# Performance work log

Measured on AMD Instinct MI355X. Metric: run time of the kernel, lower is better.

## Reference

```python
import jax, jax.numpy as jnp
import numpy as np

B, S, DN, L = 2048, 8, 8, 50        # batch, n_sparse, n_dense, hist len
V, VF = 100000, 100000              # sparse vocab, feed vocab
ED, FD = 16, 512                    # sparse embed dim, feed embed dim
HID1, HID2 = 256, 128               # DNN hidden sizes
NE, NT, EO = 8, 4, 8                # experts, tasks, expert out dim
INPUT_DIM = ED * S + DN + FD + FD   # 1160


def setup_inputs() -> dict:
    key = jax.random.key(0)
    ks = jax.random.split(key, 20)
    sc = 0.02
    f32 = jnp.float32
    return {
        "sparse_ids": jax.random.randint(ks[0], (B, S), 0, V),
        "dense": jax.random.normal(ks[1], (B, DN), f32),
        "feedid": jax.random.randint(ks[2], (B,), 0, VF),
        "hist_feedid": jax.random.randint(ks[3], (B, L), 0, VF),
        "emb_tables": jax.random.normal(ks[4], (S, V, ED), f32) * sc,
        "feed_table": jax.random.normal(ks[5], (VF, FD), f32) * sc,
        "attn_w1": jax.random.normal(ks[6], (4 * FD, 128), f32) * sc,
        "attn_b1": jnp.zeros((128,), f32),
        "attn_w2": jax.random.normal(ks[7], (128, 1), f32) * sc,
        "attn_b2": jnp.zeros((1,), f32),
        "dnn_w1": jax.random.normal(ks[8], (INPUT_DIM, HID1), f32) * sc,
        "dnn_b1": jnp.zeros((HID1,), f32),
        "dnn_w2": jax.random.normal(ks[9], (HID1, HID2), f32) * sc,
        "dnn_b2": jnp.zeros((HID2,), f32),
        "expert_w": jax.random.normal(ks[10], (NE, HID2, EO), f32) * sc,
        "gate_w": jax.random.normal(ks[11], (NT, HID2, NE), f32) * sc,
        "out_w": jax.random.normal(ks[12], (NT, EO, 1), f32) * sc,
        "out_b": jnp.zeros((NT, 1), f32),
    }


def reference(sparse_ids, dense, feedid, hist_feedid,
              emb_tables, feed_table,
              attn_w1, attn_b1, attn_w2, attn_b2,
              dnn_w1, dnn_b1, dnn_w2, dnn_b2,
              expert_w, gate_w, out_w, out_b):
    # --- sparse embeddings: one table per feature -> [B, S, ED] -> flat ---
    embed = jax.vmap(lambda t, ids: t[ids], in_axes=(0, 1), out_axes=1)(
        emb_tables, sparse_ids)                       # [B, S, ED]
    sparse_flat = embed.reshape(embed.shape[0], -1)   # [B, S*ED]

    # --- feed / history embeddings ---
    feed = feed_table[feedid]                         # [B, FD]
    hist = feed_table[hist_feedid]                    # [B, L, FD]

    # --- DIN attention (query=feed, keys=hist) ---
    q = jnp.broadcast_to(feed[:, None, :], hist.shape)          # [B, L, FD]
    x = jnp.concatenate([q, hist, q - hist, q * hist], axis=-1)  # [B, L, 4FD]
    h = jax.nn.relu(x @ attn_w1 + attn_b1)                       # [B, L, 128]
    scores = (h @ attn_w2 + attn_b2)[..., 0]                     # [B, L]
    attn = jax.nn.softmax(scores, axis=1)
    user_interest = jnp.einsum('bl,bld->bd', attn, hist)         # [B, FD]

    # --- DNN (dropout off in eval) ---
    dnn_in = jnp.concatenate([sparse_flat, dense, feed, user_interest], axis=1)
    z = jax.nn.relu(dnn_in @ dnn_w1 + dnn_b1)
    dnn_out = jax.nn.relu(z @ dnn_w2 + dnn_b2)                   # [B, 128]

    # --- MMOE (eval: no expert dropout mask) ---
    expert_out = jnp.einsum('bi,eio->beo', dnn_out, expert_w)    # [B, NE, EO]
    gates = jax.nn.softmax(jnp.einsum('bi,tie->bte', dnn_out, gate_w), axis=-1)
    task_out = jnp.einsum('bte,beo->bto', gates, expert_out)     # [B, NT, EO]

    # --- per-task heads ---
    logits = jnp.einsum('bto,toh->bth', task_out, out_w) + out_b  # [B, NT, 1]
    return jax.nn.sigmoid(logits)
```

## Files before the change

kernel.cpp:

```cpp
#include <hip/hip_runtime.h>
#include <hip/hip_bf16.h>

typedef unsigned short u16;
typedef unsigned int u32;
typedef __attribute__((ext_vector_type(8))) short short8;
typedef __attribute__((ext_vector_type(8))) u16 ushort8;
typedef __attribute__((ext_vector_type(4))) float f32x4;

#define BB 2048
#define SS 8
#define DNUM 8
#define LL 50
#define EDIM 16
#define FDIM 512
#define HID1 256
#define HID2 128
#define VF 100000
#define KDNN 1216
#define ROWS (BB*LL)

__device__ inline u16 f2bf(float x) {
    return __builtin_bit_cast(u16, __float2bfloat16(x));
}
__device__ inline float bf2f(u16 b) {
    u32 u = ((u32)b) << 16;
    return __builtin_bit_cast(float, u);
}
__device__ inline void load16_lds(const void* g, void* l) {
    __builtin_amdgcn_global_load_lds(
        (const __attribute__((address_space(1))) u32*)g,
        (__attribute__((address_space(3))) u32*)l, 16, 0, 0);
}
__device__ inline float wave_sum(float v) {
    #pragma unroll
    for (int off = 32; off > 0; off >>= 1) v += __shfl_xor(v, off, 64);
    return v;
}
__device__ inline float wave_max(float v) {
    #pragma unroll
    for (int off = 32; off > 0; off >>= 1) v = fmaxf(v, __shfl_xor(v, off, 64));
    return v;
}
__device__ inline void cvt8(const float4& a, const float4& b, ushort8& o) {
    o[0]=f2bf(a.x); o[1]=f2bf(a.y); o[2]=f2bf(a.z); o[3]=f2bf(a.w);
    o[4]=f2bf(b.x); o[5]=f2bf(b.y); o[6]=f2bf(b.z); o[7]=f2bf(b.w);
}

#define PREP_BLKS 2112
__global__ __launch_bounds__(256) void prep_small(
    const float* __restrict__ ft,
    const float* __restrict__ w1, const float* __restrict__ dw1,
    const float* __restrict__ dw2,
    u16* __restrict__ WHP_T, u16* __restrict__ WQ_T,
    u16* __restrict__ W1D_T, u16* __restrict__ W2D_T,
    const int* __restrict__ sparse_ids, const float* __restrict__ dense,
    const int* __restrict__ feedid, const float* __restrict__ emb_tables,
    u16* __restrict__ dnn_in, u16* __restrict__ A_q)
{
    int blk = blockIdx.x, t = threadIdx.x;
    if (blk < PREP_BLKS) {
        int idx = blk * 256 + t;
        if (idx < 131072) {
            int n = idx >> 10, k = idx & 1023;
            float v;
            if (k < 512) v = w1[(512 + k) * 128 + n] - w1[(1024 + k) * 128 + n];
            else         v = w1[(1024 + k) * 128 + n];
            WHP_T[n * 1024 + k] = f2bf(v);
        } else if (idx < 196608) {
            int i = idx - 131072;
            int n = i >> 9, k = i & 511;
            WQ_T[n * 512 + k] = f2bf(w1[k * 128 + n] + w1[(1024 + k) * 128 + n]);
        } else if (idx < 507904) {
            int i = idx - 196608;
            int n = i / KDNN, k = i - n * KDNN;
            W1D_T[i] = (k < 1160) ? f2bf(dw1[k * HID1 + n]) : (u16)0;
        } else if (idx < 540672) {
            int i = idx - 507904;
            int n = i >> 8, k = i & 255;
            W2D_T[i] = f2bf(dw2[k * HID2 + n]);
        }
    } else {
        int b = blk - PREP_BLKS;
        u16* drow = dnn_in + (size_t)b * KDNN;
        if (t < 128) {
            int s = t >> 4, e = t & 15;
            int id = sparse_ids[b * SS + s];
            float v = emb_tables[(size_t)s * 1600000 + (size_t)id * EDIM + e];
            drow[t] = f2bf(v);
        } else if (t < 136) {
            drow[t] = f2bf(dense[b * DNUM + (t - 128)]);
        } else if (t < 192) {
            drow[1160 + (t - 136)] = 0;
        }
        int fid = feedid[b];
        float2 f = *(const float2*)&ft[(size_t)fid * FDIM + t * 2];
        u16 u0 = f2bf(f.x), u1 = f2bf(f.y);
        drow[136 + t * 2] = u0;
        drow[136 + t * 2 + 1] = u1;
        A_q[(size_t)b * FDIM + t * 2] = u0;
        A_q[(size_t)b * FDIM + t * 2 + 1] = u1;
    }
}

template<int BM, bool RELU, bool OUT_BF16>
__global__ __launch_bounds__(256, 4) void gemm_bt(
    const u16* __restrict__ A, int lda,
    const u16* __restrict__ BT, int ldb,
    const float* __restrict__ bias,
    void* __restrict__ Cv, int M, int N, int K)
{
    constexpr int MI = BM / 32;
    __shared__ u16 As[BM * 64];
    __shared__ u16 Bs[128 * 64];
    int m0 = blockIdx.x * BM, n0 = blockIdx.y * 128;
    int tid = threadIdx.x, wave = tid >> 6, lane = tid & 63;
    int lrow = lane >> 3, lk = (lane & 7) * 8;
    f32x4 acc[MI][4];
    f32x4 zz = {0.f, 0.f, 0.f, 0.f};
    #pragma unroll
    for (int i = 0; i < MI; i++)
        #pragma unroll
        for (int j = 0; j < 4; j++) acc[i][j] = zz;
    int wm = (wave >> 1) * (BM / 2), wn = (wave & 1) * 64;

    for (int kt = 0; kt < K; kt += 64) {
        #pragma unroll
        for (int j = 0; j < MI; ++j) {
            int c = wave * MI + j;
            int row = c * 8 + lrow;
            load16_lds(A + (size_t)(m0 + row) * lda + kt + lk, &As[c * 512]);
        }
        #pragma unroll
        for (int j = 0; j < 4; ++j) {
            int c = wave * 4 + j;
            int row = c * 8 + lrow;
            load16_lds(BT + (size_t)(n0 + row) * ldb + kt + lk, &Bs[c * 512]);
        }
        __syncthreads();
        #pragma unroll
        for (int ks = 0; ks < 2; ++ks) {
            int kk = ks * 32 + (lane >> 4) * 8;
            short8 af[MI], bf[4];
            #pragma unroll
            for (int i = 0; i < MI; i++)
                af[i] = *(const short8*)&As[(wm + i * 16 + (lane & 15)) * 64 + kk];
            #pragma unroll
            for (int j = 0; j < 4; j++)
                bf[j] = *(const short8*)&Bs[(wn + j * 16 + (lane & 15)) * 64 + kk];
            #pragma unroll
            for (int i = 0; i < MI; i++)
                #pragma unroll
                for (int j = 0; j < 4; j++)
                    acc[i][j] = __builtin_amdgcn_mfma_f32_16x16x32_bf16(
                        af[i], bf[j], acc[i][j], 0, 0, 0);
        }
        __syncthreads();
    }
    #pragma unroll
    for (int i = 0; i < MI; i++) {
        #pragma unroll
        for (int j = 0; j < 4; j++) {
            #pragma unroll
            for (int r = 0; r < 4; r++) {
                int row = m0 + wm + i * 16 + (lane >> 4) * 4 + r;
                int col = n0 + wn + j * 16 + (lane & 15);
                float v = acc[i][j][r];
                if (bias) v += bias[col];
                if (RELU) v = fmaxf(v, 0.f);
                size_t off = (size_t)row * N + col;
                if (OUT_BF16) ((u16*)Cv)[off] = f2bf(v);
                else ((float*)Cv)[off] = v;
            }
        }
    }
}

#define MFMA_BF16 __builtin_amdgcn_mfma_f32_16x16x32_bf16

__global__ __launch_bounds__(256, 4) void din_fused(
    const int* __restrict__ hist_ids, const int* __restrict__ feedid,
    const float* __restrict__ ft, const u16* __restrict__ WHP_T,
    const float* __restrict__ qw, const float* __restrict__ b1,
    const float* __restrict__ w2v, u16* __restrict__ dnn_in)
{
    __shared__ float Asf[2][64 * 32];
    __shared__ u16 BsH[128 * 32];
    __shared__ u16 BsP[128 * 32];
    __shared__ u16 qls[512];
    __shared__ float qbs[128];
    __shared__ float w2s[128];
    __shared__ float sred[64 * 2];
    __shared__ float scf[64];
    __shared__ int hids[64];

    int b = blockIdx.x;
    int t = threadIdx.x, w = t >> 6, lane = t & 63;
    int fr = lane & 15, kg8 = (lane >> 4) * 8;
    int wm = (w >> 1) * 32, wn = (w & 1) * 64;
    int fid = feedid[b];

    if (t < 64) hids[t] = hist_ids[b * LL + (t < LL ? t : LL - 1)];
    if (t < 128) {
        qbs[t] = qw[b * 128 + t] + b1[t];
        w2s[t] = w2v[t];
    }
    {
        float2 qv = *(const float2*)&ft[(size_t)fid * FDIM + t * 2];
        qls[t * 2] = f2bf(qv.x);
        qls[t * 2 + 1] = f2bf(qv.y);
    }

    int srow = w * 16 + fr;
    const float* a_src0 = ft + (size_t)hist_ids[b * LL + (srow < LL ? srow : LL - 1)] * FDIM
                             + (lane >> 4) * 4;
    const float* a_src1 = a_src0 + 16;
    const u16* b_src0 = WHP_T + (size_t)(w * 32 + (lane >> 2)) * 1024 + (lane & 3) * 8;
    const u16* b_src1 = b_src0 + 16 * 1024;

    f32x4 acc[2][4];
    f32x4 zz = {0.f, 0.f, 0.f, 0.f};
    #pragma unroll
    for (int i = 0; i < 2; i++)
        #pragma unroll
        for (int j = 0; j < 4; j++) acc[i][j] = zz;

    load16_lds(a_src0,        &Asf[0][w * 512]);
    load16_lds(a_src1,        &Asf[0][w * 512 + 256]);
    load16_lds(b_src0,        &BsH[(w * 2) * 512]);
    load16_lds(b_src1,        &BsH[(w * 2 + 1) * 512]);
    load16_lds(b_src0 + 512,  &BsP[(w * 2) * 512]);
    load16_lds(b_src1 + 512,  &BsP[(w * 2 + 1) * 512]);
    load16_lds(a_src0 + 32,   &Asf[1][w * 512]);
    load16_lds(a_src1 + 32,   &Asf[1][w * 512 + 256]);
    asm volatile("s_waitcnt vmcnt(2) lgkmcnt(0)" ::: "memory");
    __builtin_amdgcn_s_barrier();

    int ws0 = wm >> 4;
    int k4a = (lane >> 4) * 2;
    int offA0 = ws0 * 512 + k4a * 64 + fr * 4;
    int offA1 = (ws0 + 1) * 512 + k4a * 64 + fr * 4;

    #pragma unroll
    for (int kt = 0; kt < 16; ++kt) {
        const int buf = kt & 1;
        const int ko = kt * 32;
        float4 h0a = *(const float4*)&Asf[buf][offA0];
        float4 h0b = *(const float4*)&Asf[buf][offA0 + 64];
        float4 h1a = *(const float4*)&Asf[buf][offA1];
        float4 h1b = *(const float4*)&Asf[buf][offA1 + 64];
        ushort8 hv0, hv1;
        cvt8(h0a, h0b, hv0);
        cvt8(h1a, h1b, hv1);
        ushort8 qv = *(const ushort8*)&qls[ko + kg8];
        short8 bh[4], bp[4];
        #pragma unroll
        for (int j = 0; j < 4; ++j) {
            int n = wn + j * 16 + fr;
            bh[j] = *(const short8*)&BsH[n * 32 + kg8];
            bp[j] = *(const short8*)&BsP[n * 32 + kg8];
        }
        short8 ah0 = __builtin_bit_cast(short8, hv0);
        short8 ah1 = __builtin_bit_cast(short8, hv1);
        #pragma unroll
        for (int j = 0; j < 4; ++j) {
            acc[0][j] = MFMA_BF16(ah0, bh[j], acc[0][j], 0, 0, 0);
            acc[1][j] = MFMA_BF16(ah1, bh[j], acc[1][j], 0, 0, 0);
        }
        ushort8 pv0, pv1;
        #pragma unroll
        for (int e = 0; e < 8; ++e) {
            pv0[e] = f2bf(bf2f(hv0[e]) * bf2f(qv[e]));
            pv1[e] = f2bf(bf2f(hv1[e]) * bf2f(qv[e]));
        }
        short8 ap0 = __builtin_bit_cast(short8, pv0);
        short8 ap1 = __builtin_bit_cast(short8, pv1);
        #pragma unroll
        for (int j = 0; j < 4; ++j) {
            acc[0][j] = MFMA_BF16(ap0, bp[j], acc[0][j], 0, 0, 0);
            acc[1][j] = MFMA_BF16(ap1, bp[j], acc[1][j], 0, 0, 0);
        }
        asm volatile("s_waitcnt lgkmcnt(0)" ::: "memory");
        __builtin_amdgcn_s_barrier();
        if (kt < 15) {
            const int knB = (kt + 1) * 32;
            load16_lds(b_src0 + knB,       &BsH[(w * 2) * 512]);
            load16_lds(b_src1 + knB,       &BsH[(w * 2 + 1) * 512]);
            load16_lds(b_src0 + 512 + knB, &BsP[(w * 2) * 512]);
            load16_lds(b_src1 + 512 + knB, &BsP[(w * 2 + 1) * 512]);
            if (kt < 14) {
                const int knA = (kt + 2) * 32;
                load16_lds(a_src0 + knA, &Asf[buf][w * 512]);
                load16_lds(a_src1 + knA, &Asf[buf][w * 512 + 256]);
                asm volatile("s_waitcnt vmcnt(2)" ::: "memory");
            } else {
                asm volatile("s_waitcnt vmcnt(0)" ::: "memory");
            }
            __builtin_amdgcn_s_barrier();
        }
    }

    #pragma unroll
    for (int i = 0; i < 2; ++i) {
        #pragma unroll
        for (int r = 0; r < 4; ++r) {
            int rl = wm + i * 16 + (lane >> 4) * 4 + r;
            float s = 0.f;
            #pragma unroll
            for (int j = 0; j < 4; ++j) {
                int col = wn + j * 16 + fr;
                float v = acc[i][j][r] + qbs[col];
                s += fmaxf(v, 0.f) * w2s[col];
            }
            s += __shfl_xor(s, 1, 64);
            s += __shfl_xor(s, 2, 64);
            s += __shfl_xor(s, 4, 64);
            s += __shfl_xor(s, 8, 64);
            if (fr == 0) sred[rl * 2 + (w & 1)] = s;
        }
    }
    __syncthreads();
    if (t < 64) scf[t] = sred[t * 2] + sred[t * 2 + 1];
    __syncthreads();
    if (w == 0) {
        float x = (lane < LL) ? scf[lane] : -1e30f;
        float mx = wave_max(x);
        float e = (lane < LL) ? __expf(x - mx) : 0.f;
        float s = wave_sum(e);
        scf[lane] = (lane < LL) ? e / s : 0.f;
    }
    __syncthreads();
    int d = t * 2;
    float a0 = 0.f, a1 = 0.f;
    #pragma unroll 5
    for (int l = 0; l < LL; ++l) {
        float2 hv = *(const float2*)&ft[(size_t)hids[l] * FDIM + d];
        float al = scf[l];
        a0 += al * hv.x;
        a1 += al * hv.y;
    }
    dnn_in[(size_t)b * KDNN + 648 + d] = f2bf(a0);
    dnn_in[(size_t)b * KDNN + 648 + d + 1] = f2bf(a1);
}

__global__ __launch_bounds__(256) void mmoe_head(
    const float* __restrict__ dnn_out, const float* __restrict__ expert_w,
    const float* __restrict__ gate_w, const float* __restrict__ out_w,
    const float* __restrict__ out_b, float* __restrict__ out)
{
    int wave = threadIdx.x >> 6, lane = threadIdx.x & 63;
    int b = blockIdx.x * 4 + wave;
    __shared__ float ds[4][128];
    __shared__ float eo[4][64];
    __shared__ float gt[4][32];
    ds[wave][lane] = dnn_out[b * 128 + lane];
    ds[wave][lane + 64] = dnn_out[b * 128 + 64 + lane];
    __syncthreads();
    int e = lane >> 3, o = lane & 7;
    float acc = 0.f;
    for (int k = 0; k < 128; ++k)
        acc += ds[wave][k] * expert_w[(e * 128 + k) * 8 + o];
    eo[wave][lane] = acc;
    if (lane < 32) {
        int tt = lane >> 3, ee = lane & 7;
        float g = 0.f;
        for (int k = 0; k < 128; ++k)
            g += ds[wave][k] * gate_w[(tt * 128 + k) * 8 + ee];
        float m = g;
        #pragma unroll
        for (int off = 4; off; off >>= 1) m = fmaxf(m, __shfl_xor(m, off, 8));
        float ex = __expf(g - m);
        float s = ex;
        #pragma unroll
        for (int off = 4; off; off >>= 1) s += __shfl_xor(s, off, 8);
        gt[wave][lane] = ex / s;
    }
    __syncthreads();
    if (lane < 32) {
        int tt = lane >> 3, o2 = lane & 7;
        float to = 0.f;
        #pragma unroll
        for (int ee = 0; ee < 8; ++ee)
            to += gt[wave][tt * 8 + ee] * eo[wave][ee * 8 + o2];
        float pl = to * out_w[tt * 8 + o2];
        #pragma unroll
        for (int off = 4; off; off >>= 1) pl += __shfl_xor(pl, off, 8);
        if (o2 == 0) {
            float logit = pl + out_b[tt];
            out[b * 4 + tt] = 1.f / (1.f + __expf(-logit));
        }
    }
}

extern "C" void kernel_launch(void* const* d_in, const int* in_sizes, int n_in,
                              void* d_out, int out_size, void* d_ws, size_t ws_size,
                              hipStream_t stream)
{
    const int*   sparse_ids = (const int*)d_in[0];
    const float* dense      = (const float*)d_in[1];
    const int*   feedid     = (const int*)d_in[2];
    const int*   hist_ids   = (const int*)d_in[3];
    const float* emb_tables = (const float*)d_in[4];
    const float* feed_table = (const float*)d_in[5];
    const float* attn_w1    = (const float*)d_in[6];
    const float* attn_b1    = (const float*)d_in[7];
    const float* attn_w2    = (const float*)d_in[8];
    const float* attn_b2    = (const float*)d_in[9];
    const float* dnn_w1     = (const float*)d_in[10];
    const float* dnn_b1     = (const float*)d_in[11];
    const float* dnn_w2     = (const float*)d_in[12];
    const float* dnn_b2     = (const float*)d_in[13];
    const float* expert_w   = (const float*)d_in[14];
    const float* gate_w     = (const float*)d_in[15];
    const float* out_w      = (const float*)d_in[16];
    const float* out_b      = (const float*)d_in[17];
    float* out = (float*)d_out;
    (void)attn_b2;

    char* ws = (char*)d_ws;
    size_t off = 0;
    auto alloc = [&](size_t bytes) {
        char* p = ws + off;
        off += (bytes + 255) & ~(size_t)255;
        return p;
    };
    u16* WHP_T = (u16*)alloc(131072 * 2);
    u16* WQ_T  = (u16*)alloc(65536 * 2);
    u16* W1D_T = (u16*)alloc((size_t)HID1 * KDNN * 2);
    u16* W2D_T = (u16*)alloc((size_t)HID2 * HID1 * 2);
    u16* AQ    = (u16*)alloc((size_t)BB * FDIM * 2);
    float* QW  = (float*)alloc((size_t)BB * 128 * 4);
    u16* DNNIN = (u16*)alloc((size_t)BB * KDNN * 2);
    u16* Z     = (u16*)alloc((size_t)BB * HID1 * 2);
    float* DOUT= (float*)alloc((size_t)BB * HID2 * 4);

    prep_small<<<PREP_BLKS + BB, 256, 0, stream>>>(
        feed_table, attn_w1, dnn_w1, dnn_w2,
        WHP_T, WQ_T, W1D_T, W2D_T,
        sparse_ids, dense, feedid, emb_tables, DNNIN, AQ);
    gemm_bt<32, false, false><<<dim3(BB / 32, 1), 256, 0, stream>>>(
        AQ, 512, WQ_T, 512, nullptr, QW, BB, 128, 512);
    din_fused<<<BB, 256, 0, stream>>>(
        hist_ids, feedid, feed_table, WHP_T, QW, attn_b1, attn_w2, DNNIN);
    gemm_bt<32, true, true><<<dim3(BB / 32, HID1 / 128), 256, 0, stream>>>(
        DNNIN, KDNN, W1D_T, KDNN, dnn_b1, Z, BB, HID1, KDNN);
    gemm_bt<32, true, false><<<dim3(BB / 32, 1), 256, 0, stream>>>(
        Z, HID1, W2D_T, HID1, dnn_b2, DOUT, BB, HID2, HID1);
    mmoe_head<<<BB / 4, 256, 0, stream>>>(DOUT, expert_w, gate_w, out_w,
                                          out_b, out);
}
```

Measured before the change: 138.7 us.

## Swizzle DIN weight layout for LDS banks and halve GEMM N-tile

```diff
diff --git a/kernel.cpp b/kernel.cpp
--- a/kernel.cpp
+++ b/kernel.cpp
@@ -51,7 +51,7 @@
     const float* __restrict__ ft,
     const float* __restrict__ w1, const float* __restrict__ dw1,
     const float* __restrict__ dw2,
-    u16* __restrict__ WHP_T, u16* __restrict__ WQ_T,
+    u16* __restrict__ WHP_S, u16* __restrict__ WQ_T,
     u16* __restrict__ W1D_T, u16* __restrict__ W2D_T,
     const int* __restrict__ sparse_ids, const float* __restrict__ dense,
     const int* __restrict__ feedid, const float* __restrict__ emb_tables,
@@ -65,7 +65,8 @@
             float v;
             if (k < 512) v = w1[(512 + k) * 128 + n] - w1[(1024 + k) * 128 + n];
             else         v = w1[(1024 + k) * 128 + n];
-            WHP_T[n * 1024 + k] = f2bf(v);
+            int ks = (k & ~31) | ((k & 31) ^ ((n & 3) << 3));
+            WHP_S[n * 1024 + ks] = f2bf(v);
         } else if (idx < 196608) {
             int i = idx - 131072;
             int n = i >> 9, k = i & 511;
@@ -102,7 +103,7 @@
     }
 }
 
-template<int BM, bool RELU, bool OUT_BF16>
+template<int BM, int BN, bool RELU, bool OUT_BF16>
 __global__ __launch_bounds__(256, 4) void gemm_bt(
     const u16* __restrict__ A, int lda,
     const u16* __restrict__ BT, int ldb,
@@ -110,18 +111,19 @@
     void* __restrict__ Cv, int M, int N, int K)
 {
     constexpr int MI = BM / 32;
+    constexpr int NJ = BN / 32;
     __shared__ u16 As[BM * 64];
-    __shared__ u16 Bs[128 * 64];
-    int m0 = blockIdx.x * BM, n0 = blockIdx.y * 128;
+    __shared__ u16 Bs[BN * 64];
+    int m0 = blockIdx.x * BM, n0 = blockIdx.y * BN;
     int tid = threadIdx.x, wave = tid >> 6, lane = tid & 63;
     int lrow = lane >> 3, lk = (lane & 7) * 8;
-    f32x4 acc[MI][4];
+    f32x4 acc[MI][NJ];
     f32x4 zz = {0.f, 0.f, 0.f, 0.f};
     #pragma unroll
     for (int i = 0; i < MI; i++)
         #pragma unroll
-        for (int j = 0; j < 4; j++) acc[i][j] = zz;
-    int wm = (wave >> 1) * (BM / 2), wn = (wave & 1) * 64;
+        for (int j = 0; j < NJ; j++) acc[i][j] = zz;
+    int wm = (wave >> 1) * (BM / 2), wn = (wave & 1) * (BN / 2);
 
     for (int kt = 0; kt < K; kt += 64) {
         #pragma unroll
@@ -131,8 +133,8 @@
             load16_lds(A + (size_t)(m0 + row) * lda + kt + lk, &As[c * 512]);
         }
         #pragma unroll
-        for (int j = 0; j < 4; ++j) {
-            int c = wave * 4 + j;
+        for (int j = 0; j < NJ; ++j) {
+            int c = wave * NJ + j;
             int row = c * 8 + lrow;
             load16_lds(BT + (size_t)(n0 + row) * ldb + kt + lk, &Bs[c * 512]);
         }
@@ -140,17 +142,17 @@
         #pragma unroll
         for (int ks = 0; ks < 2; ++ks) {
             int kk = ks * 32 + (lane >> 4) * 8;
-            short8 af[MI], bf[4];
+            short8 af[MI], bf[NJ];
             #pragma unroll
             for (int i = 0; i < MI; i++)
                 af[i] = *(const short8*)&As[(wm + i * 16 + (lane & 15)) * 64 + kk];
             #pragma unroll
-            for (int j = 0; j < 4; j++)
+            for (int j = 0; j < NJ; j++)
                 bf[j] = *(const short8*)&Bs[(wn + j * 16 + (lane & 15)) * 64 + kk];
             #pragma unroll
             for (int i = 0; i < MI; i++)
                 #pragma unroll
-                for (int j = 0; j < 4; j++)
+                for (int j = 0; j < NJ; j++)
                     acc[i][j] = __builtin_amdgcn_mfma_f32_16x16x32_bf16(
                         af[i], bf[j], acc[i][j], 0, 0, 0);
         }
@@ -159,7 +161,7 @@
     #pragma unroll
     for (int i = 0; i < MI; i++) {
         #pragma unroll
-        for (int j = 0; j < 4; j++) {
+        for (int j = 0; j < NJ; j++) {
             #pragma unroll
             for (int r = 0; r < 4; r++) {
                 int row = m0 + wm + i * 16 + (lane >> 4) * 4 + r;
@@ -179,7 +181,7 @@
 
 __global__ __launch_bounds__(256, 4) void din_fused(
     const int* __restrict__ hist_ids, const int* __restrict__ feedid,
-    const float* __restrict__ ft, const u16* __restrict__ WHP_T,
+    const float* __restrict__ ft, const u16* __restrict__ WHP_S,
     const float* __restrict__ qw, const float* __restrict__ b1,
     const float* __restrict__ w2v, u16* __restrict__ dnn_in)
 {
@@ -214,7 +216,7 @@
     const float* a_src0 = ft + (size_t)hist_ids[b * LL + (srow < LL ? srow : LL - 1)] * FDIM
                              + (lane >> 4) * 4;
     const float* a_src1 = a_src0 + 16;
-    const u16* b_src0 = WHP_T + (size_t)(w * 32 + (lane >> 2)) * 1024 + (lane & 3) * 8;
+    const u16* b_src0 = WHP_S + (size_t)(w * 32 + (lane >> 2)) * 1024 + (lane & 3) * 8;
     const u16* b_src1 = b_src0 + 16 * 1024;
 
     f32x4 acc[2][4];
@@ -256,8 +258,9 @@
         #pragma unroll
         for (int j = 0; j < 4; ++j) {
             int n = wn + j * 16 + fr;
-            bh[j] = *(const short8*)&BsH[n * 32 + kg8];
-            bp[j] = *(const short8*)&BsP[n * 32 + kg8];
+            int kk = kg8 ^ ((n & 3) << 3);
+            bh[j] = *(const short8*)&BsH[n * 32 + kk];
+            bp[j] = *(const short8*)&BsP[n * 32 + kk];
         }
         short8 ah0 = __builtin_bit_cast(short8, hv0);
         short8 ah1 = __builtin_bit_cast(short8, hv1);
@@ -423,7 +426,7 @@
         off += (bytes + 255) & ~(size_t)255;
         return p;
     };
-    u16* WHP_T = (u16*)alloc(131072 * 2);
+    u16* WHP_S = (u16*)alloc(131072 * 2);
     u16* WQ_T  = (u16*)alloc(65536 * 2);
     u16* W1D_T = (u16*)alloc((size_t)HID1 * KDNN * 2);
     u16* W2D_T = (u16*)alloc((size_t)HID2 * HID1 * 2);
@@ -435,15 +438,15 @@
 
     prep_small<<<PREP_BLKS + BB, 256, 0, stream>>>(
         feed_table, attn_w1, dnn_w1, dnn_w2,
-        WHP_T, WQ_T, W1D_T, W2D_T,
+        WHP_S, WQ_T, W1D_T, W2D_T,
         sparse_ids, dense, feedid, emb_tables, DNNIN, AQ);
-    gemm_bt<32, false, false><<<dim3(BB / 32, 1), 256, 0, stream>>>(
+    gemm_bt<32, 64, false, false><<<dim3(BB / 32, 2), 256, 0, stream>>>(
         AQ, 512, WQ_T, 512, nullptr, QW, BB, 128, 512);
     din_fused<<<BB, 256, 0, stream>>>(
-        hist_ids, feedid, feed_table, WHP_T, QW, attn_b1, attn_w2, DNNIN);
-    gemm_bt<32, true, true><<<dim3(BB / 32, HID1 / 128), 256, 0, stream>>>(
+        hist_ids, feedid, feed_table, WHP_S, QW, attn_b1, attn_w2, DNNIN);
+    gemm_bt<32, 64, true, true><<<dim3(BB / 32, HID1 / 64), 256, 0, stream>>>(
         DNNIN, KDNN, W1D_T, KDNN, dnn_b1, Z, BB, HID1, KDNN);
-    gemm_bt<32, true, false><<<dim3(BB / 32, 1), 256, 0, stream>>>(
+    gemm_bt<32, 64, true, false><<<dim3(BB / 32, HID2 / 64), 256, 0, stream>>>(
         Z, HID1, W2D_T, HID1, dnn_b2, DOUT, BB, HID2, HID1);
     mmoe_head<<<BB / 4, 256, 0, stream>>>(DOUT, expert_w, gate_w, out_w,
                                           out_b, out);
```

Measured after the change: 131.7 us. -5.0%, faster.
